# Kernel tuning notes

Hardware: AMD Instinct MI355X
Metric: run time of the kernel (lower is better)

Reference implementation:

```python
import jax, jax.numpy as jnp
import numpy as np

N, E, F, G, C, L = 20000, 320000, 75, 64, 10, 5
EPS = 1e-5


def setup_inputs():
    key = jax.random.key(0)
    ks = jax.random.split(key, 16)
    x = jax.random.normal(ks[0], (N, 6), jnp.float32)
    edge_index = jax.random.randint(ks[1], (2, E), 0, N, dtype=jnp.int32)
    batch = jnp.sort(jax.random.randint(ks[2], (N,), 0, G, dtype=jnp.int32))
    gcn_w = jax.random.normal(ks[3], (6, F), jnp.float32) / np.sqrt(6.0)
    gcn_b = jnp.zeros((F,), jnp.float32)
    pre_w = jax.random.normal(ks[4], (L, 2 * F, F), jnp.float32) / np.sqrt(2.0 * F)
    pre_b = jnp.zeros((L, F), jnp.float32)
    post_w = jax.random.normal(ks[5], (L, 13 * F, F), jnp.float32) / np.sqrt(13.0 * F)
    post_b = jnp.zeros((L, F), jnp.float32)
    lin_w = jax.random.normal(ks[6], (L, F, F), jnp.float32) / np.sqrt(1.0 * F)
    lin_b = jnp.zeros((L, F), jnp.float32)
    bn_g = jnp.ones((L, F), jnp.float32)
    bn_b = jnp.zeros((L, F), jnp.float32)
    w1 = jax.random.normal(ks[7], (F, 50), jnp.float32) / np.sqrt(1.0 * F)
    b1 = jnp.zeros((50,), jnp.float32)
    w2 = jax.random.normal(ks[8], (50, 25), jnp.float32) / np.sqrt(50.0)
    b2 = jnp.zeros((25,), jnp.float32)
    w3 = jax.random.normal(ks[9], (25, C), jnp.float32) / np.sqrt(25.0)
    b3 = jnp.zeros((C,), jnp.float32)
    return dict(x=x, edge_index=edge_index, batch=batch, gcn_w=gcn_w, gcn_b=gcn_b,
                pre_w=pre_w, pre_b=pre_b, post_w=post_w, post_b=post_b,
                lin_w=lin_w, lin_b=lin_b, bn_g=bn_g, bn_b=bn_b,
                w1=w1, b1=b1, w2=w2, b2=b2, w3=w3, b3=b3)


def reference(x, edge_index, batch, gcn_w, gcn_b, pre_w, pre_b, post_w, post_b,
              lin_w, lin_b, bn_g, bn_b, w1, b1, w2, b2, w3, b3):
    row, col = edge_index[0], edge_index[1]  # messages flow row (j) -> col (i)
    ones_e = jnp.ones((E,), jnp.float32)

    # ---- GCNConv(6, 75) with self-loops and symmetric normalization ----
    xw = x @ gcn_w                                   # [N, F]
    deg = jax.ops.segment_sum(ones_e, col, N) + 1.0  # in-degree + self-loop
    dinv = 1.0 / jnp.sqrt(deg)
    norm_e = (dinv[row] * dinv[col])[:, None]        # [E, 1]
    h = jax.ops.segment_sum(norm_e * xw[row], col, N) + (dinv * dinv)[:, None] * xw + gcn_b

    # ---- degree-based scalers (shared by all PNA layers) ----
    cnt = jax.ops.segment_sum(ones_e, col, N)        # in-degree per node
    avg_log = jnp.mean(jnp.log(cnt + 1.0))           # avg_deg['log'] from this graph's degree histogram
    d = jnp.maximum(cnt, 1.0)
    amp = (jnp.log(d + 1.0) / avg_log)[:, None]      # amplification
    att = (avg_log / jnp.log(d + 1.0))[:, None]      # attenuation
    cnt_c = jnp.maximum(cnt, 1.0)[:, None]
    has_nb = (cnt > 0)[:, None]

    for l in range(L):
        # pre-MLP on [x_i, x_j] per edge
        m = jnp.concatenate([h[col], h[row]], axis=-1) @ pre_w[l] + pre_b[l]  # [E, F]
        s = jax.ops.segment_sum(m, col, N)
        mean = s / cnt_c
        mean_sq = jax.ops.segment_sum(m * m, col, N) / cnt_c
        std = jnp.sqrt(jax.nn.relu(mean_sq - mean * mean) + EPS)
        mn = jnp.where(has_nb, jax.ops.segment_min(m, col, N), 0.0)
        mx = jnp.where(has_nb, jax.ops.segment_max(m, col, N), 0.0)
        agg = jnp.concatenate([mean, mn, mx, std], axis=-1)          # [N, 4F]
        scaled = jnp.concatenate([agg, agg * amp, agg * att], -1)    # [N, 12F]
        o = jnp.concatenate([h, scaled], axis=-1) @ post_w[l] + post_b[l]  # post-MLP
        o = o @ lin_w[l] + lin_b[l]                                  # final lin
        mu = o.mean(axis=0)
        var = o.var(axis=0)
        o = (o - mu) / jnp.sqrt(var + EPS) * bn_g[l] + bn_b[l]       # BatchNorm (batch stats)
        h = jax.nn.relu(o)

    # ---- global_add_pool + MLP (dropout = identity in eval) ----
    g = jax.ops.segment_sum(h, batch, G)
    g = jax.nn.relu(g @ w1 + b1)
    g = jax.nn.relu(g @ w2 + b2)
    return g @ w3 + b3  # [G, C]
```

## Files before the change

### kernel.cpp

```cpp
#include <hip/hip_runtime.h>
#include <hip/hip_bf16.h>

#define NN 20000
#define EE 320000
#define FF 75
#define GG 64
#define LL 5
#define EPS 1e-5f

#define KUV 96
#define NUV 160
#define KPOST 384
#define NPOST 240
#define KLIN 96

typedef short bf16x8 __attribute__((ext_vector_type(8)));
typedef float f32x4 __attribute__((ext_vector_type(4)));

__device__ inline void gAtomicAdd(float* p, float v) { unsafeAtomicAdd(p, v); }

__device__ inline ushort f2bs(float x) {
    __hip_bfloat16 b = __float2bfloat16(x);
    return *(ushort*)&b;
}

__device__ inline float bs2f(ushort u) {
    unsigned int x = ((unsigned int)u) << 16;
    return __uint_as_float(x);
}


__global__ void count_kernel(const int* __restrict__ col, int* __restrict__ cnt, int E) {
    int e = blockIdx.x * blockDim.x + threadIdx.x;
    if (e < E) atomicAdd(&cnt[col[e]], 1);
}

__global__ void partial_kernel(const int* __restrict__ cnt, int* __restrict__ bsum, int N) {
    __shared__ int sh[256];
    int tid = threadIdx.x;
    int i = blockIdx.x * 256 + tid;
    sh[tid] = (i < N) ? cnt[i] : 0;
    __syncthreads();
    for (int s = 128; s > 0; s >>= 1) {
        if (tid < s) sh[tid] += sh[tid + s];
        __syncthreads();
    }
    if (tid == 0) bsum[blockIdx.x] = sh[0];
}

__global__ void scanb_kernel(const int* __restrict__ bsum, int* __restrict__ bbase,
                             int* __restrict__ offs, int NB) {
    __shared__ int sh[128];
    int tid = threadIdx.x;
    int v = (tid < NB) ? bsum[tid] : 0;
    sh[tid] = v;
    __syncthreads();
    for (int d = 1; d < 128; d <<= 1) {
        int t = (tid >= d) ? sh[tid - d] : 0;
        __syncthreads();
        sh[tid] += t;
        __syncthreads();
    }
    if (tid < NB) bbase[tid] = sh[tid] - v;
    if (tid == 0) offs[NN] = EE;
}

__global__ void offs_kernel(const int* __restrict__ cnt, const int* __restrict__ bbase,
                            int* __restrict__ offs, int* __restrict__ cursor, int N) {
    __shared__ int sh[256];
    int tid = threadIdx.x;
    int i = blockIdx.x * 256 + tid;
    int v = (i < N) ? cnt[i] : 0;
    sh[tid] = v;
    __syncthreads();
    for (int d = 1; d < 256; d <<= 1) {
        int t = (tid >= d) ? sh[tid - d] : 0;
        __syncthreads();
        sh[tid] += t;
        __syncthreads();
    }
    int excl = sh[tid] - v + bbase[blockIdx.x];
    if (i < N) { offs[i] = excl; cursor[i] = excl; }
}

__global__ void fill_kernel(const int* __restrict__ row, const int* __restrict__ col,
                            int* __restrict__ cursor, int* __restrict__ csr, int E) {
    int e = blockIdx.x * blockDim.x + threadIdx.x;
    if (e < E) {
        int c = col[e];
        int pos = atomicAdd(&cursor[c], 1);
        csr[pos] = row[e];
    }
}


__global__ void dinv_kernel(const int* __restrict__ cnt, float* __restrict__ dinv,
                            float* __restrict__ scal, int N) {
    __shared__ float red[256];
    int i = blockIdx.x * 256 + threadIdx.x;
    float lg = 0.f;
    if (i < N) {
        float c = (float)cnt[i];
        dinv[i] = 1.f / sqrtf(c + 1.f);
        lg = logf(c + 1.f);
    }
    red[threadIdx.x] = lg;
    __syncthreads();
    for (int s = 128; s > 0; s >>= 1) {
        if (threadIdx.x < s) red[threadIdx.x] += red[threadIdx.x + s];
        __syncthreads();
    }
    if (threadIdx.x == 0) gAtomicAdd(&scal[0], red[0]);
}


__global__ void xw_kernel(const float* __restrict__ x, const float* __restrict__ gw,
                          float* __restrict__ xw, int N) {
    int idx = blockIdx.x * 256 + threadIdx.x;
    if (idx >= N * FF) return;
    int n = idx / FF, f = idx % FF;
    float acc = 0.f;
#pragma unroll
    for (int k = 0; k < 6; k++) acc += x[n * 6 + k] * gw[k * FF + f];
    xw[idx] = acc;
}

__global__ void gcn_kernel(const float* __restrict__ xw, const float* __restrict__ dinv,
                           const int* __restrict__ offs, const int* __restrict__ csr,
                           const float* __restrict__ gcn_b, const int* __restrict__ cnt,
                           const float* __restrict__ scal,
                           float* __restrict__ o2,
                           float* __restrict__ amp, float* __restrict__ att, int N) {
    int i = blockIdx.x;
    int t = threadIdx.x;
    int s0 = offs[i], s1 = offs[i + 1];
    float di = dinv[i];
    if (t < FF) {
        float acc = 0.f;
        int k = s0;
        for (; k + 1 < s1; k += 2) {
            int r0 = csr[k], r1 = csr[k + 1];
            acc += dinv[r0] * xw[r0 * FF + t] + dinv[r1] * xw[r1 * FF + t];
        }
        if (k < s1) {
            int r = csr[k];
            acc += dinv[r] * xw[r * FF + t];
        }
        o2[(size_t)i * 80 + t] = di * acc + di * di * xw[i * FF + t] + gcn_b[t];
    }
    if (t == 0) {
        float al = scal[0] / (float)N;
        float d = fmaxf((float)cnt[i], 1.f);
        float lg = logf(d + 1.f);
        amp[i] = lg / al;
        att[i] = al / lg;
    }
}


#define S_UV (LL * NUV * KUV)
#define S_POST (LL * NPOST * KPOST)
#define S_LIN (LL * 80 * KLIN)

__global__ void prep_bt_kernel(const float* __restrict__ pre_w, const float* __restrict__ pre_b,
                               const float* __restrict__ post_w, const float* __restrict__ lin_w,
                               ushort* __restrict__ BTuv, ushort* __restrict__ BTpost,
                               ushort* __restrict__ BTlin) {
    int idx = blockIdx.x * 256 + threadIdx.x;
    if (idx < S_UV) {
        int l = idx / (NUV * KUV);
        int r = idx % (NUV * KUV);
        int c = r / KUV, k = r % KUV;
        float v = 0.f;
        if (k < FF) {
            if (c < FF) v = pre_w[((size_t)l * 150 + k) * FF + c];
            else if (c >= 80 && c < 80 + FF) v = pre_w[((size_t)l * 150 + FF + k) * FF + (c - 80)];
        } else if (k == FF && c < FF) {
            v = pre_b[l * FF + c];
        }
        BTuv[idx] = f2bs(v);
    } else if (idx < S_UV + S_POST) {
        int j = idx - S_UV;
        int l = j / (NPOST * KPOST);
        int r = j % (NPOST * KPOST);
        int c = r / KPOST, k = r % KPOST;
        float v = 0.f;
        if (k < FF) {
            if (c < FF) v = post_w[((size_t)l * 975 + k) * FF + c];
        } else if (k < 375) {
            if (c < FF) v = post_w[((size_t)l * 975 + k) * FF + c];
            else if (c >= 80 && c < 80 + FF) v = post_w[((size_t)l * 975 + k + 300) * FF + (c - 80)];
            else if (c >= 160 && c < 160 + FF) v = post_w[((size_t)l * 975 + k + 600) * FF + (c - 160)];
        }
        BTpost[j] = f2bs(v);
    } else if (idx < S_UV + S_POST + S_LIN) {
        int j = idx - S_UV - S_POST;
        int l = j / (80 * KLIN);
        int r = j % (80 * KLIN);
        int c = r / KLIN, k = r % KLIN;
        float v = (c < FF && k < FF) ? lin_w[((size_t)l * FF + k) * FF + c] : 0.f;
        BTlin[j] = f2bs(v);
    }
}


__global__ __launch_bounds__(64) void uv_bn_kernel(
    const float* __restrict__ o2, const float* __restrict__ ss, int apply_bn,
    const ushort* __restrict__ BT, float* __restrict__ U, ushort* __restrict__ Vb,
    ushort* __restrict__ hagg) {
    int lane = threadIdx.x;
    int col16 = lane & 15, quad = lane >> 4;
    int n = blockIdx.x * 16 + col16;
    const float* orow = o2 + (size_t)n * 80;
    const ushort* bbase = BT + (size_t)col16 * KUV + quad * 8;

    f32x4 acc[10];
#pragma unroll
    for (int i = 0; i < 10; i++) acc[i] = (f32x4){0.f, 0.f, 0.f, 0.f};

#pragma unroll
    for (int kt = 0; kt < 3; kt++) {
        int kb = kt * 32 + quad * 8;
        bf16x8 af;
        if (kb < 80) {
            float4 v0 = *(const float4*)(orow + kb);
            float4 v1 = *(const float4*)(orow + kb + 4);
            float vv[8] = {v0.x, v0.y, v0.z, v0.w, v1.x, v1.y, v1.z, v1.w};
#pragma unroll
            for (int j = 0; j < 8; j++) {
                int k = kb + j;
                float v = vv[j];
                if (apply_bn) v = fmaxf(v * ss[k] + ss[80 + k], 0.f);
                ushort b = (k < FF) ? f2bs(v) : (k == FF ? (ushort)0x3F80 : (ushort)0);
                af[j] = (short)b;
            }
            if (kb < FF) {
                *(bf16x8*)(hagg + (size_t)n * KPOST + kb) = af;
            }
        } else {
            af = (bf16x8){0, 0, 0, 0, 0, 0, 0, 0};
        }
#pragma unroll
        for (int nt = 0; nt < 10; nt++) {
            bf16x8 bfr = *(const bf16x8*)(bbase + nt * (16 * KUV) + kt * 32);
            acc[nt] = __builtin_amdgcn_mfma_f32_16x16x32_bf16(af, bfr, acc[nt], 0, 0, 0);
        }
    }
    int n0 = blockIdx.x * 16;
#pragma unroll
    for (int nt = 0; nt < 10; nt++) {
        int col = nt * 16 + col16;
#pragma unroll
        for (int r = 0; r < 4; r++) {
            int nn = n0 + quad * 4 + r;
            if (col < FF) U[(size_t)nn * 80 + col] = acc[nt][r];
            else if (col >= 80 && col < 80 + FF) Vb[(size_t)nn * 80 + (col - 80)] = f2bs(acc[nt][r]);
        }
    }
}


__global__ __launch_bounds__(64) void post_lin_kernel(
    const ushort* __restrict__ A, const ushort* __restrict__ BT,
    const ushort* __restrict__ BL, const float* __restrict__ amp,
    const float* __restrict__ att, float* __restrict__ o2,
    float* __restrict__ slots) {
    __shared__ __align__(16) ushort olds[16 * 104];
    int lane = threadIdx.x;
    int col16 = lane & 15, quad = lane >> 4;
    int n0 = blockIdx.x * 16;
    const ushort* arow = A + (size_t)(n0 + col16) * KPOST + quad * 8;
    const ushort* bbase = BT + (size_t)col16 * KPOST + quad * 8;

    f32x4 acc[15];
#pragma unroll
    for (int i = 0; i < 15; i++) acc[i] = (f32x4){0.f, 0.f, 0.f, 0.f};

#pragma unroll 2
    for (int kt = 0; kt < 12; kt++) {
        bf16x8 af = *(const bf16x8*)(arow + kt * 32);
#pragma unroll
        for (int nt = 0; nt < 15; nt++) {
            bf16x8 bfr = *(const bf16x8*)(bbase + nt * (16 * KPOST) + kt * 32);
            acc[nt] = __builtin_amdgcn_mfma_f32_16x16x32_bf16(af, bfr, acc[nt], 0, 0, 0);
        }
    }
    float ampv[4], attv[4];
#pragma unroll
    for (int r = 0; r < 4; r++) {
        int n = n0 + quad * 4 + r;
        ampv[r] = amp[n];
        attv[r] = att[n];
    }
#pragma unroll
    for (int g = 0; g < 5; g++) {
        int col = g * 16 + col16;
#pragma unroll
        for (int r = 0; r < 4; r++) {
            float ov = acc[g][r] + ampv[r] * acc[g + 5][r] + attv[r] * acc[g + 10][r];
            olds[(quad * 4 + r) * 104 + col] = (col < FF) ? f2bs(ov) : (ushort)0;
        }
    }
    *(ushort4*)(olds + (lane >> 2) * 104 + 80 + (lane & 3) * 4) = (ushort4){0, 0, 0, 0};
    __syncthreads();

    f32x4 acc2[5];
#pragma unroll
    for (int i = 0; i < 5; i++) acc2[i] = (f32x4){0.f, 0.f, 0.f, 0.f};
    const ushort* blbase = BL + (size_t)col16 * KLIN + quad * 8;
#pragma unroll
    for (int kt = 0; kt < 3; kt++) {
        bf16x8 af = *(const bf16x8*)(olds + col16 * 104 + kt * 32 + quad * 8);
#pragma unroll
        for (int nt = 0; nt < 5; nt++) {
            bf16x8 bfr = *(const bf16x8*)(blbase + nt * (16 * KLIN) + kt * 32);
            acc2[nt] = __builtin_amdgcn_mfma_f32_16x16x32_bf16(af, bfr, acc2[nt], 0, 0, 0);
        }
    }
    float* slot = slots + (blockIdx.x & 31) * 160;
#pragma unroll
    for (int nt = 0; nt < 5; nt++) {
        int col = nt * 16 + col16;
        float s = 0.f, q = 0.f;
#pragma unroll
        for (int r = 0; r < 4; r++) {
            int n = n0 + quad * 4 + r;
            float v = acc2[nt][r];
            if (col < FF) {
                o2[(size_t)n * 80 + col] = v;
                s += v;
                q += v * v;
            }
        }
        s += __shfl_xor(s, 16); s += __shfl_xor(s, 32);
        q += __shfl_xor(q, 16); q += __shfl_xor(q, 32);
        if (lane < 16 && col < FF) {
            gAtomicAdd(&slot[col], s);
            gAtomicAdd(&slot[80 + col], q);
        }
    }
}

__global__ void stats_reduce_kernel(const float* __restrict__ slots,
                                    const float* __restrict__ bg, const float* __restrict__ bb,
                                    float* __restrict__ ss) {
    int c = threadIdx.x;
    if (c >= FF) return;
    float su = 0.f, sq = 0.f;
    for (int s = 0; s < 32; s++) {
        su += slots[s * 160 + c];
        sq += slots[s * 160 + 80 + c];
    }
    float mu = su * (1.f / (float)NN);
    float var = sq * (1.f / (float)NN) - mu * mu;
    float scale = bg[c] * rsqrtf(var + EPS);
    ss[c] = scale;
    ss[80 + c] = bb[c] - mu * scale;
}


__global__ __launch_bounds__(64) void edge_agg_kernel(
    const float* __restrict__ U, const ushort* __restrict__ V,
    const int* __restrict__ offs, const int* __restrict__ csr,
    const int* __restrict__ cnt, ushort* __restrict__ hagg) {
    int i = blockIdx.x;
    int lane = threadIdx.x;
    int s0 = offs[i], s1 = offs[i + 1];
    bool two = lane < 11;
    float ui1 = U[(size_t)i * 80 + lane];
    float ui2 = two ? U[(size_t)i * 80 + 64 + lane] : 0.f;
    float s1a = 0.f, ss1 = 0.f, mn1 = 1e30f, mx1 = -1e30f;
    float s2a = 0.f, ss2 = 0.f, mn2 = 1e30f, mx2 = -1e30f;
    int k = s0;
    for (; k + 1 < s1; k += 2) {
        int r0 = csr[k], r1 = csr[k + 1];
        float a0 = ui1 + bs2f(V[(size_t)r0 * 80 + lane]);
        float a1 = ui1 + bs2f(V[(size_t)r1 * 80 + lane]);
        s1a += a0 + a1;
        ss1 += a0 * a0 + a1 * a1;
        mn1 = fminf(mn1, fminf(a0, a1));
        mx1 = fmaxf(mx1, fmaxf(a0, a1));
        if (two) {
            float b0 = ui2 + bs2f(V[(size_t)r0 * 80 + 64 + lane]);
            float b1 = ui2 + bs2f(V[(size_t)r1 * 80 + 64 + lane]);
            s2a += b0 + b1;
            ss2 += b0 * b0 + b1 * b1;
            mn2 = fminf(mn2, fminf(b0, b1));
            mx2 = fmaxf(mx2, fmaxf(b0, b1));
        }
    }
    if (k < s1) {
        int r0 = csr[k];
        float a0 = ui1 + bs2f(V[(size_t)r0 * 80 + lane]);
        s1a += a0; ss1 += a0 * a0;
        mn1 = fminf(mn1, a0); mx1 = fmaxf(mx1, a0);
        if (two) {
            float b0 = ui2 + bs2f(V[(size_t)r0 * 80 + 64 + lane]);
            s2a += b0; ss2 += b0 * b0;
            mn2 = fminf(mn2, b0); mx2 = fmaxf(mx2, b0);
        }
    }
    int c = cnt[i];
    float cc = fmaxf((float)c, 1.f);
    ushort* a = hagg + (size_t)i * KPOST + FF;
    {
        float mean = s1a / cc;
        float stdv = sqrtf(fmaxf(ss1 / cc - mean * mean, 0.f) + EPS);
        if (c == 0) { mn1 = 0.f; mx1 = 0.f; }
        a[lane] = f2bs(mean);
        a[FF + lane] = f2bs(mn1);
        a[2 * FF + lane] = f2bs(mx1);
        a[3 * FF + lane] = f2bs(stdv);
    }
    if (two) {
        int t = 64 + lane;
        float mean = s2a / cc;
        float stdv = sqrtf(fmaxf(ss2 / cc - mean * mean, 0.f) + EPS);
        if (c == 0) { mn2 = 0.f; mx2 = 0.f; }
        a[t] = f2bs(mean);
        a[FF + t] = f2bs(mn2);
        a[2 * FF + t] = f2bs(mx2);
        a[3 * FF + t] = f2bs(stdv);
    }
    if (lane < 9) hagg[(size_t)i * KPOST + 375 + lane] = 0;
}


__global__ void pool_kernel(const float* __restrict__ o2, const float* __restrict__ ss,
                            const int* __restrict__ batch, float* __restrict__ g, int N) {
    __shared__ float acc[GG * FF];
    int n0 = blockIdx.x * 64;
    int n1 = min(n0 + 64, N);
    if (n0 >= N) return;
    int g0 = batch[n0];
    int g1 = batch[n1 - 1];
    int range = g1 - g0 + 1;
    for (int i = threadIdx.x; i < range * FF; i += 256) acc[i] = 0.f;
    __syncthreads();
    int rows = n1 - n0;
    for (int idx = threadIdx.x; idx < rows * FF; idx += 256) {
        int r = idx / FF, c = idx % FF;
        int n = n0 + r;
        float val = fmaxf(o2[(size_t)n * 80 + c] * ss[c] + ss[80 + c], 0.f);
        gAtomicAdd(&acc[(batch[n] - g0) * FF + c], val);
    }
    __syncthreads();
    for (int i = threadIdx.x; i < range * FF; i += 256) gAtomicAdd(&g[g0 * FF + i], acc[i]);
}

__global__ void mlp_kernel(const float* __restrict__ g,
                           const float* __restrict__ w1, const float* __restrict__ b1,
                           const float* __restrict__ w2, const float* __restrict__ b2,
                           const float* __restrict__ w3, const float* __restrict__ b3,
                           float* __restrict__ out) {
    __shared__ float gr[FF], h1[50], h2[25];
    int gi = blockIdx.x, t = threadIdx.x;
    for (int j = t; j < FF; j += 64) gr[j] = g[gi * FF + j];
    __syncthreads();
    if (t < 50) {
        float a = b1[t];
        for (int k = 0; k < FF; k++) a += gr[k] * w1[k * 50 + t];
        h1[t] = fmaxf(a, 0.f);
    }
    __syncthreads();
    if (t < 25) {
        float a = b2[t];
        for (int k = 0; k < 50; k++) a += h1[k] * w2[k * 25 + t];
        h2[t] = fmaxf(a, 0.f);
    }
    __syncthreads();
    if (t < 10) {
        float a = b3[t];
        for (int k = 0; k < 25; k++) a += h2[k] * w3[k * 10 + t];
        out[gi * 10 + t] = a;
    }
}


extern "C" void kernel_launch(void* const* d_in, const int* in_sizes, int n_in,
                              void* d_out, int out_size, void* d_ws, size_t ws_size,
                              hipStream_t stream) {
    const float* x = (const float*)d_in[0];
    const int* ei = (const int*)d_in[1];
    const int* batch = (const int*)d_in[2];
    const float* gcn_w = (const float*)d_in[3];
    const float* gcn_b = (const float*)d_in[4];
    const float* pre_w = (const float*)d_in[5];
    const float* pre_b = (const float*)d_in[6];
    const float* post_w = (const float*)d_in[7];
    const float* lin_w = (const float*)d_in[9];
    const float* bn_g = (const float*)d_in[11];
    const float* bn_b = (const float*)d_in[12];
    const float* w1 = (const float*)d_in[13];
    const float* b1 = (const float*)d_in[14];
    const float* w2 = (const float*)d_in[15];
    const float* b2 = (const float*)d_in[16];
    const float* w3 = (const float*)d_in[17];
    const float* b3 = (const float*)d_in[18];
    float* out = (float*)d_out;

    const int* row = ei;
    const int* col = ei + EE;

    char* ws = (char*)d_ws;
    size_t off = 0;
    auto alloc = [&](size_t bytes) {
        char* p = ws + off;
        off += (bytes + 255) & ~(size_t)255;
        return p;
    };
    int* cnt = (int*)alloc(NN * 4);
    int* offs = (int*)alloc((NN + 1) * 4);
    int* cursor = (int*)alloc(NN * 4);
    int* csr = (int*)alloc(EE * 4);
    int* bsum = (int*)alloc(128 * 4);
    int* bbase = (int*)alloc(128 * 4);
    float* dinv = (float*)alloc(NN * 4);
    float* amp = (float*)alloc(NN * 4);
    float* att = (float*)alloc(NN * 4);
    float* scal = (float*)alloc((1 + LL * 160 + LL * 32 * 160) * 4);
    float* ssbase = scal + 1;
    float* slotbase = scal + 1 + LL * 160;
    float* o2 = (float*)alloc((size_t)NN * 80 * 4);
    float* ubuf = (float*)alloc((size_t)NN * 80 * 4);
    ushort* vbuf = (ushort*)alloc((size_t)NN * 80 * 2);
    ushort* hagg = (ushort*)alloc((size_t)NN * KPOST * 2);
    ushort* BTuv = (ushort*)alloc((size_t)S_UV * 2);
    ushort* BTpost = (ushort*)alloc((size_t)S_POST * 2);
    ushort* BTlin = (ushort*)alloc((size_t)S_LIN * 2);
    float* gbuf = (float*)alloc(GG * FF * 4);

    hipMemsetAsync(cnt, 0, NN * 4, stream);
    hipMemsetAsync(scal, 0, (1 + LL * 160 + LL * 32 * 160) * 4, stream);
    hipMemsetAsync(gbuf, 0, GG * FF * 4, stream);

    const int B = 256;
    const int NB = (NN + 255) / 256;
    count_kernel<<<(EE + B - 1) / B, B, 0, stream>>>(col, cnt, EE);
    dinv_kernel<<<NB, B, 0, stream>>>(cnt, dinv, scal, NN);
    partial_kernel<<<NB, B, 0, stream>>>(cnt, bsum, NN);
    scanb_kernel<<<1, 128, 0, stream>>>(bsum, bbase, offs, NB);
    offs_kernel<<<NB, B, 0, stream>>>(cnt, bbase, offs, cursor, NN);
    fill_kernel<<<(EE + B - 1) / B, B, 0, stream>>>(row, col, cursor, csr, EE);
    xw_kernel<<<(NN * FF + B - 1) / B, B, 0, stream>>>(x, gcn_w, ubuf, NN);
    gcn_kernel<<<NN, 128, 0, stream>>>(ubuf, dinv, offs, csr, gcn_b, cnt, scal,
                                       o2, amp, att, NN);
    {
        int tot = S_UV + S_POST + S_LIN;
        prep_bt_kernel<<<(tot + B - 1) / B, B, 0, stream>>>(pre_w, pre_b, post_w, lin_w,
                                                            BTuv, BTpost, BTlin);
    }

    const int GS = NN / 16;
    for (int l = 0; l < LL; l++) {
        float* ss_prev = ssbase + (l - 1) * 160;
        float* ss_cur = ssbase + l * 160;
        float* slots = slotbase + l * 32 * 160;

        uv_bn_kernel<<<GS, 64, 0, stream>>>(o2, (l == 0) ? ssbase : ss_prev, (l > 0) ? 1 : 0,
                                            BTuv + (size_t)l * NUV * KUV, ubuf, vbuf, hagg);
        edge_agg_kernel<<<NN, 64, 0, stream>>>(ubuf, vbuf, offs, csr, cnt, hagg);
        post_lin_kernel<<<GS, 64, 0, stream>>>(hagg, BTpost + (size_t)l * NPOST * KPOST,
                                               BTlin + (size_t)l * 80 * KLIN, amp, att,
                                               o2, slots);
        stats_reduce_kernel<<<1, 128, 0, stream>>>(slots, bn_g + l * FF, bn_b + l * FF, ss_cur);
    }

    pool_kernel<<<(NN + 63) / 64, 256, 0, stream>>>(o2, ssbase + (LL - 1) * 160, batch, gbuf, NN);
    mlp_kernel<<<GG, 64, 0, stream>>>(gbuf, w1, b1, w2, b2, w3, b3, out);
}
```

Measured before the change: 529.0 us.

## Fuse BN stats reduction into consumers; bf16 pre-scaled GCN gather and paired-lane edge aggregation

Removes the per-layer single-block stats_reduce kernel by having each uv_bn and pool block recompute the batch-norm scale/shift from the slot partials into shared memory. The GCN input is now pre-scaled by dinv and stored as bf16, so the gather reads half the bytes and skips per-neighbour dinv lookups. Both the GCN and edge aggregation kernels now have each lane handle two adjacent features with ushort2 loads on 40 lanes, instead of a ragged 64+11 split. The trade-off is redundant stats recomputation in every block and bf16 rounding in the GCN aggregation.

```diff
diff --git a/kernel.cpp b/kernel.cpp
--- a/kernel.cpp
+++ b/kernel.cpp
@@ -114,41 +114,54 @@
 }
 
 
-__global__ void xw_kernel(const float* __restrict__ x, const float* __restrict__ gw,
-                          float* __restrict__ xw, int N) {
+__global__ void xs_kernel(const float* __restrict__ x, const float* __restrict__ gw,
+                          const float* __restrict__ dinv, ushort* __restrict__ xs, int N) {
     int idx = blockIdx.x * 256 + threadIdx.x;
-    if (idx >= N * FF) return;
-    int n = idx / FF, f = idx % FF;
-    float acc = 0.f;
-#pragma unroll
-    for (int k = 0; k < 6; k++) acc += x[n * 6 + k] * gw[k * FF + f];
-    xw[idx] = acc;
-}
-
-__global__ void gcn_kernel(const float* __restrict__ xw, const float* __restrict__ dinv,
-                           const int* __restrict__ offs, const int* __restrict__ csr,
-                           const float* __restrict__ gcn_b, const int* __restrict__ cnt,
-                           const float* __restrict__ scal,
-                           float* __restrict__ o2,
-                           float* __restrict__ amp, float* __restrict__ att, int N) {
-    int i = blockIdx.x;
-    int t = threadIdx.x;
-    int s0 = offs[i], s1 = offs[i + 1];
-    float di = dinv[i];
+    if (idx >= N * 80) return;
+    int n = idx / 80, t = idx % 80;
+    float v = 0.f;
     if (t < FF) {
         float acc = 0.f;
+#pragma unroll
+        for (int k = 0; k < 6; k++) acc += x[n * 6 + k] * gw[k * FF + t];
+        v = dinv[n] * acc;
+    }
+    xs[idx] = f2bs(v);
+}
+
+__global__ __launch_bounds__(64) void gcn_kernel(
+    const ushort* __restrict__ xs, const float* __restrict__ dinv,
+    const int* __restrict__ offs, const int* __restrict__ csr,
+    const float* __restrict__ gcn_b, const int* __restrict__ cnt,
+    const float* __restrict__ scal, float* __restrict__ o2,
+    float* __restrict__ amp, float* __restrict__ att, int N) {
+    int i = blockIdx.x;
+    int lane = threadIdx.x;
+    int s0 = offs[i], s1 = offs[i + 1];
+    if (lane < 40) {
+        float a0 = 0.f, a1 = 0.f;
         int k = s0;
         for (; k + 1 < s1; k += 2) {
             int r0 = csr[k], r1 = csr[k + 1];
-            acc += dinv[r0] * xw[r0 * FF + t] + dinv[r1] * xw[r1 * FF + t];
+            ushort2 v0 = *(const ushort2*)(xs + (size_t)r0 * 80 + 2 * lane);
+            ushort2 v1 = *(const ushort2*)(xs + (size_t)r1 * 80 + 2 * lane);
+            a0 += bs2f(v0.x) + bs2f(v1.x);
+            a1 += bs2f(v0.y) + bs2f(v1.y);
         }
         if (k < s1) {
-            int r = csr[k];
-            acc += dinv[r] * xw[r * FF + t];
-        }
-        o2[(size_t)i * 80 + t] = di * acc + di * di * xw[i * FF + t] + gcn_b[t];
-    }
-    if (t == 0) {
+            int r0 = csr[k];
+            ushort2 v0 = *(const ushort2*)(xs + (size_t)r0 * 80 + 2 * lane);
+            a0 += bs2f(v0.x);
+            a1 += bs2f(v0.y);
+        }
+        ushort2 vs = *(const ushort2*)(xs + (size_t)i * 80 + 2 * lane);
+        a0 += bs2f(vs.x);
+        a1 += bs2f(vs.y);
+        float di = dinv[i];
+        int t0 = 2 * lane, t1 = 2 * lane + 1;
+        if (t0 < FF) o2[(size_t)i * 80 + t0] = di * a0 + gcn_b[t0];
+        if (t1 < FF) o2[(size_t)i * 80 + t1] = di * a1 + gcn_b[t1];
+    } else if (lane == 63) {
         float al = scal[0] / (float)N;
         float d = fmaxf((float)cnt[i], 1.f);
         float lg = logf(d + 1.f);
@@ -205,14 +218,38 @@
 
 
 __global__ __launch_bounds__(64) void uv_bn_kernel(
-    const float* __restrict__ o2, const float* __restrict__ ss, int apply_bn,
+    const float* __restrict__ o2, const float* __restrict__ slots,
+    const float* __restrict__ bg, const float* __restrict__ bb, int apply_bn,
     const ushort* __restrict__ BT, float* __restrict__ U, ushort* __restrict__ Vb,
     ushort* __restrict__ hagg) {
+    __shared__ float ssL[160];
     int lane = threadIdx.x;
     int col16 = lane & 15, quad = lane >> 4;
     int n = blockIdx.x * 16 + col16;
     const float* orow = o2 + (size_t)n * 80;
     const ushort* bbase = BT + (size_t)col16 * KUV + quad * 8;
+
+    if (apply_bn) {
+        for (int c = lane; c < 80; c += 64) {
+            if (c < FF) {
+                float su = 0.f, sq = 0.f;
+#pragma unroll 8
+                for (int s = 0; s < 32; s++) {
+                    su += slots[s * 160 + c];
+                    sq += slots[s * 160 + 80 + c];
+                }
+                float mu = su * (1.f / (float)NN);
+                float var = sq * (1.f / (float)NN) - mu * mu;
+                float sc = bg[c] * rsqrtf(var + EPS);
+                ssL[c] = sc;
+                ssL[80 + c] = bb[c] - mu * sc;
+            } else {
+                ssL[c] = 0.f;
+                ssL[80 + c] = 0.f;
+            }
+        }
+        __syncthreads();
+    }
 
     f32x4 acc[10];
 #pragma unroll
@@ -230,7 +267,7 @@
             for (int j = 0; j < 8; j++) {
                 int k = kb + j;
                 float v = vv[j];
-                if (apply_bn) v = fmaxf(v * ss[k] + ss[80 + k], 0.f);
+                if (apply_bn) v = fmaxf(v * ssL[k] + ssL[80 + k], 0.f);
                 ushort b = (k < FF) ? f2bs(v) : (k == FF ? (ushort)0x3F80 : (ushort)0);
                 af[j] = (short)b;
             }
@@ -341,23 +378,6 @@
     }
 }
 
-__global__ void stats_reduce_kernel(const float* __restrict__ slots,
-                                    const float* __restrict__ bg, const float* __restrict__ bb,
-                                    float* __restrict__ ss) {
-    int c = threadIdx.x;
-    if (c >= FF) return;
-    float su = 0.f, sq = 0.f;
-    for (int s = 0; s < 32; s++) {
-        su += slots[s * 160 + c];
-        sq += slots[s * 160 + 80 + c];
-    }
-    float mu = su * (1.f / (float)NN);
-    float var = sq * (1.f / (float)NN) - mu * mu;
-    float scale = bg[c] * rsqrtf(var + EPS);
-    ss[c] = scale;
-    ss[80 + c] = bb[c] - mu * scale;
-}
-
 
 __global__ __launch_bounds__(64) void edge_agg_kernel(
     const float* __restrict__ U, const ushort* __restrict__ V,
@@ -366,86 +386,104 @@
     int i = blockIdx.x;
     int lane = threadIdx.x;
     int s0 = offs[i], s1 = offs[i + 1];
-    bool two = lane < 11;
-    float ui1 = U[(size_t)i * 80 + lane];
-    float ui2 = two ? U[(size_t)i * 80 + 64 + lane] : 0.f;
-    float s1a = 0.f, ss1 = 0.f, mn1 = 1e30f, mx1 = -1e30f;
-    float s2a = 0.f, ss2 = 0.f, mn2 = 1e30f, mx2 = -1e30f;
-    int k = s0;
-    for (; k + 1 < s1; k += 2) {
-        int r0 = csr[k], r1 = csr[k + 1];
-        float a0 = ui1 + bs2f(V[(size_t)r0 * 80 + lane]);
-        float a1 = ui1 + bs2f(V[(size_t)r1 * 80 + lane]);
-        s1a += a0 + a1;
-        ss1 += a0 * a0 + a1 * a1;
-        mn1 = fminf(mn1, fminf(a0, a1));
-        mx1 = fmaxf(mx1, fmaxf(a0, a1));
-        if (two) {
-            float b0 = ui2 + bs2f(V[(size_t)r0 * 80 + 64 + lane]);
-            float b1 = ui2 + bs2f(V[(size_t)r1 * 80 + 64 + lane]);
-            s2a += b0 + b1;
-            ss2 += b0 * b0 + b1 * b1;
-            mn2 = fminf(mn2, fminf(b0, b1));
-            mx2 = fmaxf(mx2, fmaxf(b0, b1));
-        }
-    }
-    if (k < s1) {
-        int r0 = csr[k];
-        float a0 = ui1 + bs2f(V[(size_t)r0 * 80 + lane]);
-        s1a += a0; ss1 += a0 * a0;
-        mn1 = fminf(mn1, a0); mx1 = fmaxf(mx1, a0);
-        if (two) {
-            float b0 = ui2 + bs2f(V[(size_t)r0 * 80 + 64 + lane]);
-            s2a += b0; ss2 += b0 * b0;
-            mn2 = fminf(mn2, b0); mx2 = fmaxf(mx2, b0);
-        }
-    }
-    int c = cnt[i];
-    float cc = fmaxf((float)c, 1.f);
-    ushort* a = hagg + (size_t)i * KPOST + FF;
-    {
-        float mean = s1a / cc;
-        float stdv = sqrtf(fmaxf(ss1 / cc - mean * mean, 0.f) + EPS);
-        if (c == 0) { mn1 = 0.f; mx1 = 0.f; }
-        a[lane] = f2bs(mean);
-        a[FF + lane] = f2bs(mn1);
-        a[2 * FF + lane] = f2bs(mx1);
-        a[3 * FF + lane] = f2bs(stdv);
-    }
-    if (two) {
-        int t = 64 + lane;
-        float mean = s2a / cc;
-        float stdv = sqrtf(fmaxf(ss2 / cc - mean * mean, 0.f) + EPS);
-        if (c == 0) { mn2 = 0.f; mx2 = 0.f; }
-        a[t] = f2bs(mean);
-        a[FF + t] = f2bs(mn2);
-        a[2 * FF + t] = f2bs(mx2);
-        a[3 * FF + t] = f2bs(stdv);
-    }
-    if (lane < 9) hagg[(size_t)i * KPOST + 375 + lane] = 0;
-}
-
-
-__global__ void pool_kernel(const float* __restrict__ o2, const float* __restrict__ ss,
+    if (lane < 40) {
+        float2 uiv = *(const float2*)(U + (size_t)i * 80 + 2 * lane);
+        float ui0 = uiv.x, ui1 = uiv.y;
+        float sa0 = 0.f, sq0 = 0.f, mn0 = 1e30f, mx0 = -1e30f;
+        float sa1 = 0.f, sq1 = 0.f, mn1 = 1e30f, mx1 = -1e30f;
+        int k = s0;
+        for (; k + 1 < s1; k += 2) {
+            int r0 = csr[k], r1 = csr[k + 1];
+            ushort2 v0 = *(const ushort2*)(V + (size_t)r0 * 80 + 2 * lane);
+            ushort2 v1 = *(const ushort2*)(V + (size_t)r1 * 80 + 2 * lane);
+            float a0 = ui0 + bs2f(v0.x), b0 = ui0 + bs2f(v1.x);
+            float a1 = ui1 + bs2f(v0.y), b1 = ui1 + bs2f(v1.y);
+            sa0 += a0 + b0; sq0 += a0 * a0 + b0 * b0;
+            mn0 = fminf(mn0, fminf(a0, b0)); mx0 = fmaxf(mx0, fmaxf(a0, b0));
+            sa1 += a1 + b1; sq1 += a1 * a1 + b1 * b1;
+            mn1 = fminf(mn1, fminf(a1, b1)); mx1 = fmaxf(mx1, fmaxf(a1, b1));
+        }
+        if (k < s1) {
+            int r0 = csr[k];
+            ushort2 v0 = *(const ushort2*)(V + (size_t)r0 * 80 + 2 * lane);
+            float a0 = ui0 + bs2f(v0.x);
+            float a1 = ui1 + bs2f(v0.y);
+            sa0 += a0; sq0 += a0 * a0; mn0 = fminf(mn0, a0); mx0 = fmaxf(mx0, a0);
+            sa1 += a1; sq1 += a1 * a1; mn1 = fminf(mn1, a1); mx1 = fmaxf(mx1, a1);
+        }
+        int c = cnt[i];
+        float cc = fmaxf((float)c, 1.f);
+        ushort* a = hagg + (size_t)i * KPOST + FF;
+        int t0 = 2 * lane, t1 = 2 * lane + 1;
+        {
+            float mean = sa0 / cc;
+            float stdv = sqrtf(fmaxf(sq0 / cc - mean * mean, 0.f) + EPS);
+            if (c == 0) { mn0 = 0.f; mx0 = 0.f; }
+            if (t0 < FF) {
+                a[t0] = f2bs(mean);
+                a[FF + t0] = f2bs(mn0);
+                a[2 * FF + t0] = f2bs(mx0);
+                a[3 * FF + t0] = f2bs(stdv);
+            }
+        }
+        {
+            float mean = sa1 / cc;
+            float stdv = sqrtf(fmaxf(sq1 / cc - mean * mean, 0.f) + EPS);
+            if (c == 0) { mn1 = 0.f; mx1 = 0.f; }
+            if (t1 < FF) {
+                a[t1] = f2bs(mean);
+                a[FF + t1] = f2bs(mn1);
+                a[2 * FF + t1] = f2bs(mx1);
+                a[3 * FF + t1] = f2bs(stdv);
+            }
+        }
+    } else if (lane >= 48 && lane < 57) {
+        hagg[(size_t)i * KPOST + 375 + (lane - 48)] = 0;
+    }
+}
+
+
+__global__ void pool_kernel(const float* __restrict__ o2, const float* __restrict__ slots,
+                            const float* __restrict__ bg, const float* __restrict__ bb,
                             const int* __restrict__ batch, float* __restrict__ g, int N) {
     __shared__ float acc[GG * FF];
+    __shared__ float ssL[160];
+    int tid = threadIdx.x;
     int n0 = blockIdx.x * 64;
     int n1 = min(n0 + 64, N);
     if (n0 >= N) return;
+    for (int c = tid; c < 80; c += 256) {
+        if (c < FF) {
+            float su = 0.f, sq = 0.f;
+#pragma unroll 8
+            for (int s = 0; s < 32; s++) {
+                su += slots[s * 160 + c];
+                sq += slots[s * 160 + 80 + c];
+            }
+            float mu = su * (1.f / (float)NN);
+            float var = sq * (1.f / (float)NN) - mu * mu;
+            float sc = bg[c] * rsqrtf(var + EPS);
+            ssL[c] = sc;
+            ssL[80 + c] = bb[c] - mu * sc;
+        } else {
+            ssL[c] = 0.f;
+            ssL[80 + c] = 0.f;
+        }
+    }
     int g0 = batch[n0];
     int g1 = batch[n1 - 1];
     int range = g1 - g0 + 1;
-    for (int i = threadIdx.x; i < range * FF; i += 256) acc[i] = 0.f;
+    for (int i = tid; i < range * FF; i += 256) acc[i] = 0.f;
     __syncthreads();
     int rows = n1 - n0;
-    for (int idx = threadIdx.x; idx < rows * FF; idx += 256) {
+    for (int idx = tid; idx < rows * FF; idx += 256) {
         int r = idx / FF, c = idx % FF;
         int n = n0 + r;
-        float val = fmaxf(o2[(size_t)n * 80 + c] * ss[c] + ss[80 + c], 0.f);
+        float val = fmaxf(o2[(size_t)n * 80 + c] * ssL[c] + ssL[80 + c], 0.f);
         gAtomicAdd(&acc[(batch[n] - g0) * FF + c], val);
     }
     __syncthreads();
-    for (int i = threadIdx.x; i < range * FF; i += 256) gAtomicAdd(&g[g0 * FF + i], acc[i]);
+    for (int i = tid; i < range * FF; i += 256) gAtomicAdd(&g[g0 * FF + i], acc[i]);
 }
 
 __global__ void mlp_kernel(const float* __restrict__ g,
@@ -518,9 +556,8 @@
     float* dinv = (float*)alloc(NN * 4);
     float* amp = (float*)alloc(NN * 4);
     float* att = (float*)alloc(NN * 4);
-    float* scal = (float*)alloc((1 + LL * 160 + LL * 32 * 160) * 4);
-    float* ssbase = scal + 1;
-    float* slotbase = scal + 1 + LL * 160;
+    float* scal = (float*)alloc((1 + LL * 32 * 160) * 4);
+    float* slotbase = scal + 1;
     float* o2 = (float*)alloc((size_t)NN * 80 * 4);
     float* ubuf = (float*)alloc((size_t)NN * 80 * 4);
     ushort* vbuf = (ushort*)alloc((size_t)NN * 80 * 2);
@@ -531,7 +568,7 @@
     float* gbuf = (float*)alloc(GG * FF * 4);
 
     hipMemsetAsync(cnt, 0, NN * 4, stream);
-    hipMemsetAsync(scal, 0, (1 + LL * 160 + LL * 32 * 160) * 4, stream);
+    hipMemsetAsync(scal, 0, (1 + LL * 32 * 160) * 4, stream);
     hipMemsetAsync(gbuf, 0, GG * FF * 4, stream);
 
     const int B = 256;
@@ -542,9 +579,9 @@
     scanb_kernel<<<1, 128, 0, stream>>>(bsum, bbase, offs, NB);
     offs_kernel<<<NB, B, 0, stream>>>(cnt, bbase, offs, cursor, NN);
     fill_kernel<<<(EE + B - 1) / B, B, 0, stream>>>(row, col, cursor, csr, EE);
-    xw_kernel<<<(NN * FF + B - 1) / B, B, 0, stream>>>(x, gcn_w, ubuf, NN);
-    gcn_kernel<<<NN, 128, 0, stream>>>(ubuf, dinv, offs, csr, gcn_b, cnt, scal,
-                                       o2, amp, att, NN);
+    xs_kernel<<<(NN * 80 + B - 1) / B, B, 0, stream>>>(x, gcn_w, dinv, vbuf, NN);
+    gcn_kernel<<<NN, 64, 0, stream>>>(vbuf, dinv, offs, csr, gcn_b, cnt, scal,
+                                      o2, amp, att, NN);
     {
         int tot = S_UV + S_POST + S_LIN;
         prep_bt_kernel<<<(tot + B - 1) / B, B, 0, stream>>>(pre_w, pre_b, post_w, lin_w,
@@ -553,19 +590,21 @@
 
     const int GS = NN / 16;
     for (int l = 0; l < LL; l++) {
-        float* ss_prev = ssbase + (l - 1) * 160;
-        float* ss_cur = ssbase + l * 160;
+        float* slots_prev = slotbase + (l - 1) * 32 * 160;
         float* slots = slotbase + l * 32 * 160;
-
-        uv_bn_kernel<<<GS, 64, 0, stream>>>(o2, (l == 0) ? ssbase : ss_prev, (l > 0) ? 1 : 0,
+        int lp = (l > 0) ? (l - 1) : 0;
+
+        uv_bn_kernel<<<GS, 64, 0, stream>>>(o2, (l == 0) ? slotbase : slots_prev,
+                                            bn_g + lp * FF, bn_b + lp * FF, (l > 0) ? 1 : 0,
                                             BTuv + (size_t)l * NUV * KUV, ubuf, vbuf, hagg);
         edge_agg_kernel<<<NN, 64, 0, stream>>>(ubuf, vbuf, offs, csr, cnt, hagg);
         post_lin_kernel<<<GS, 64, 0, stream>>>(hagg, BTpost + (size_t)l * NPOST * KPOST,
                                                BTlin + (size_t)l * 80 * KLIN, amp, att,
                                                o2, slots);
-        stats_reduce_kernel<<<1, 128, 0, stream>>>(slots, bn_g + l * FF, bn_b + l * FF, ss_cur);
-    }
-
-    pool_kernel<<<(NN + 63) / 64, 256, 0, stream>>>(o2, ssbase + (LL - 1) * 160, batch, gbuf, NN);
+    }
+
+    pool_kernel<<<(NN + 63) / 64, 256, 0, stream>>>(o2, slotbase + (LL - 1) * 32 * 160,
+                                                    bn_g + (LL - 1) * FF, bn_b + (LL - 1) * FF,
+                                                    batch, gbuf, NN);
     mlp_kernel<<<GG, 64, 0, stream>>>(gbuf, w1, b1, w2, b2, w3, b3, out);
 }
```

After: 509.8 us. -3.6%, faster.
